# Kernel tuning notes

Measured on AMD Instinct MI355X. Metric: run time of the kernel, lower is better.

The kernel has to match this reference:

```python
import jax, jax.numpy as jnp
import numpy as np
import math

D_MODEL = 1024
NUM_HEADS = 16
HEAD_DIM = D_MODEL // NUM_HEADS  # 64
THETA = 10000.0
BATCH = 2
SEQ = 2048


def setup_inputs() -> dict:
    key = jax.random.key(0)
    ks = jax.random.split(key, 5)
    scale = 0.02
    return {
        "in_features": jax.random.normal(ks[0], (BATCH, SEQ, D_MODEL), jnp.float32),
        "q_proj": jax.random.normal(ks[1], (D_MODEL, D_MODEL), jnp.float32) * scale,
        "k_proj": jax.random.normal(ks[2], (D_MODEL, D_MODEL), jnp.float32) * scale,
        "v_proj": jax.random.normal(ks[3], (D_MODEL, D_MODEL), jnp.float32) * scale,
        "o_proj": jax.random.normal(ks[4], (D_MODEL, D_MODEL), jnp.float32) * scale,
        "token_positions": jnp.arange(SEQ, dtype=jnp.int32),
    }


def _rope(x, token_positions):
    # x: [b, h, s, head_dim]; interleaved even/odd rotation
    half = HEAD_DIM // 2
    inv_freq = 1.0 / (THETA ** (2.0 * jnp.arange(half, dtype=x.dtype) / HEAD_DIM))
    angle = token_positions.astype(x.dtype)[:, None] * inv_freq[None, :]  # [s, half]
    cos, sin = jnp.cos(angle), jnp.sin(angle)
    x_e, x_o = x[..., ::2], x[..., 1::2]
    r_e = x_e * cos - x_o * sin
    r_o = x_e * sin + x_o * cos
    # interleave back: [..., s, half, 2] -> [..., s, head_dim]
    return jnp.stack([r_e, r_o], axis=-1).reshape(x.shape)


def reference(in_features, q_proj, k_proj, v_proj, o_proj, token_positions):
    b, s, _ = in_features.shape
    # projections: weight layout is [d_out, d_in]
    Q = jnp.einsum('bsd,kd->bsk', in_features, q_proj)
    K = jnp.einsum('bsd,kd->bsk', in_features, k_proj)
    V = jnp.einsum('bsd,kd->bsk', in_features, v_proj)
    # split heads: [b, h, s, head_dim]
    Q = Q.reshape(b, s, NUM_HEADS, HEAD_DIM).transpose(0, 2, 1, 3)
    K = K.reshape(b, s, NUM_HEADS, HEAD_DIM).transpose(0, 2, 1, 3)
    V = V.reshape(b, s, NUM_HEADS, HEAD_DIM).transpose(0, 2, 1, 3)
    Q = _rope(Q, token_positions)
    K = _rope(K, token_positions)
    scores = jnp.einsum('bhnd,bhmd->bhnm', Q, K) / math.sqrt(HEAD_DIM)
    causal = jnp.tril(jnp.ones((s, s), dtype=bool))  # [s, s]
    scores = jnp.where(causal[None, None], scores, -jnp.inf)
    attn = jax.nn.softmax(scores, axis=-1)
    out = jnp.einsum('bhnm,bhmd->bhnd', attn, V)
    out = out.transpose(0, 2, 1, 3).reshape(b, s, D_MODEL)
    return jnp.einsum('bsv,dv->bsd', out, o_proj)
```

## Files before the change

kernel.cpp:

```cpp
#include <hip/hip_runtime.h>
#include <hip/hip_bf16.h>

#define D_MODEL 1024
#define NHEAD   16
#define HDIM    64
#define SEQQ    2048
#define NBATCH  2
#define MROWS   (NBATCH * SEQQ)

typedef unsigned short u16;
typedef __attribute__((ext_vector_type(8))) short short8;
typedef __attribute__((ext_vector_type(4))) short bf16x4;
typedef __attribute__((ext_vector_type(4))) float floatx4;

__device__ __forceinline__ u16 f2b(float f) {
    union { __hip_bfloat16 h; u16 u; } cv;
    cv.h = __float2bfloat16(f);
    return cv.u;
}
__device__ __forceinline__ float b2f(u16 u) {
    return __uint_as_float(((unsigned int)u) << 16);
}
__device__ __forceinline__ short8 load8(const u16* p) {
    return *reinterpret_cast<const short8*>(p);
}
__device__ __forceinline__ bf16x4 load4v(const u16* p) {
    return *reinterpret_cast<const bf16x4*>(p);
}
__device__ __forceinline__ unsigned pack2(float lo, float hi) {
    return ((unsigned)f2b(hi) << 16) | (unsigned)f2b(lo);
}
__device__ __forceinline__ void async_cp16(const void* g, void* l) {
    __builtin_amdgcn_global_load_lds(
        (const __attribute__((address_space(1))) void*)g,
        (__attribute__((address_space(3))) void*)l, 16, 0, 0);
}

__global__ void cvt_all(const float* __restrict__ X,
                        const float* __restrict__ w0, const float* __restrict__ w1,
                        const float* __restrict__ w2, const float* __restrict__ w3,
                        const int* __restrict__ pos,
                        u16* __restrict__ xo,
                        u16* __restrict__ o0, u16* __restrict__ o1,
                        u16* __restrict__ o2, u16* __restrict__ o3,
                        float2* __restrict__ tab) {
    const int z = blockIdx.y;
    const int i = blockIdx.x * 256 + threadIdx.x;
    if (z == 8) {
        if (i < SEQQ * 32) {
            const int j = i >> 11, s = i & (SEQQ - 1);
            const float p = (float)pos[s];
            const float inv = expf(-(float)j * (9.210340371976184f / 32.0f));
            float sn, cs;
            sincosf(p * inv, &sn, &cs);
            tab[i] = make_float2(cs, sn);
        }
        return;
    }
    const int n4 = (D_MODEL * D_MODEL) / 4;
    const float* in;
    u16* out;
    if (z < 4) { in = X + (size_t)z * n4 * 4;  out = xo + (size_t)z * n4 * 4; }
    else {
        in  = (z == 4) ? w0 : (z == 5) ? w1 : (z == 6) ? w2 : w3;
        out = (z == 4) ? o0 : (z == 5) ? o1 : (z == 6) ? o2 : o3;
    }
    int src = i;
    if (z == 4 || z == 5) {
        const int orow = i >> 8;
        const int g    = i & 255;
        const int irow = (orow & ~63) | (((orow & 31) << 1) | ((orow >> 5) & 1));
        src = irow * 256 + g;
    }
    float4 v = reinterpret_cast<const float4*>(in)[src];
    ushort4 o;
    o.x = f2b(v.x); o.y = f2b(v.y); o.z = f2b(v.z); o.w = f2b(v.w);
    reinterpret_cast<ushort4*>(out)[i] = o;
}

__global__ __launch_bounds__(256) void gemm_qkv(
    const u16* __restrict__ A,
    const u16* __restrict__ B0, const u16* __restrict__ B1, const u16* __restrict__ B2,
    u16* __restrict__ Qt, u16* __restrict__ Kt, u16* __restrict__ Vt,
    const float2* __restrict__ tab)
{
    const int K = D_MODEL;
    const int z = blockIdx.z;
    const u16* Bt = (z == 0) ? B0 : (z == 1 ? B1 : B2);

    __shared__ __attribute__((aligned(16))) u16 As[2][128 * 32];
    __shared__ __attribute__((aligned(16))) u16 Bs[2][128 * 32];

    const int tid  = threadIdx.x;
    const int w    = tid >> 6;
    const int lane = tid & 63;
    const int l15  = lane & 15;
    const int quad = lane >> 4;
    const int wm   = w >> 1, wn = w & 1;
    const int tm   = blockIdx.x * 128, tn = blockIdx.y * 128;

    floatx4 acc[4][4];
#pragma unroll
    for (int i = 0; i < 4; i++)
#pragma unroll
        for (int j = 0; j < 4; j++) {
            floatx4 zz = {0.f, 0.f, 0.f, 0.f};
            acc[i][j] = zz;
        }

    const int srow = lane >> 2;
    const int scol = (lane & 3) * 8;

    auto stage = [&](int buf, int k0) {
#pragma unroll
        for (int ch = w; ch < 8; ch += 4) {
            async_cp16(A  + (size_t)(tm + ch * 16 + srow) * K + k0 + scol, &As[buf][ch * 512]);
            async_cp16(Bt + (size_t)(tn + ch * 16 + srow) * K + k0 + scol, &Bs[buf][ch * 512]);
        }
    };

    stage(0, 0);

    for (int kt = 0; kt < 32; ++kt) {
        asm volatile("s_waitcnt vmcnt(0)" ::: "memory");
        __builtin_amdgcn_s_barrier();
        if (kt < 31) stage((kt + 1) & 1, (kt + 1) * 32);

        const u16* AsB = &As[kt & 1][0];
        const u16* BsB = &Bs[kt & 1][0];

        short8 af[4], bfr[4];
#pragma unroll
        for (int mi = 0; mi < 4; mi++)
            af[mi] = load8(&AsB[(wm * 64 + mi * 16 + l15) * 32 + quad * 8]);
#pragma unroll
        for (int ni = 0; ni < 4; ni++)
            bfr[ni] = load8(&BsB[(wn * 64 + ni * 16 + l15) * 32 + quad * 8]);
#pragma unroll
        for (int mi = 0; mi < 4; mi++)
#pragma unroll
            for (int ni = 0; ni < 4; ni++)
                acc[mi][ni] = __builtin_amdgcn_mfma_f32_16x16x32_bf16(af[mi], bfr[ni], acc[mi][ni], 0, 0, 0);
        __builtin_amdgcn_s_barrier();
    }

    if (z == 2) {
#pragma unroll
        for (int mi = 0; mi < 4; mi++) {
            const int r0 = tm + wm * 64 + mi * 16 + quad * 4;
            const int bb = r0 >> 11, s0 = r0 & (SEQQ - 1);
#pragma unroll
            for (int ni = 0; ni < 4; ni++) {
                const int colb = tn + wn * 64 + ni * 16 + l15;
                const int d = colb & 63, hh = colb >> 6;
                ushort4 pk;
                pk.x = f2b(acc[mi][ni][0]);
                pk.y = f2b(acc[mi][ni][1]);
                pk.z = f2b(acc[mi][ni][2]);
                pk.w = f2b(acc[mi][ni][3]);
                *reinterpret_cast<ushort4*>(
                    &Vt[(((size_t)(bb * NHEAD + hh)) * HDIM + d) * SEQQ + s0]) = pk;
            }
        }
    } else {
        const float qsc = (z == 0) ? 0.18033688011112042f : 1.0f;
        u16* Outp = (z == 0) ? Qt : Kt;
#pragma unroll
        for (int mi = 0; mi < 4; mi++) {
            const int r0 = tm + wm * 64 + mi * 16 + quad * 4;
            const int bb = r0 >> 11, s0 = r0 & (SEQQ - 1);
#pragma unroll
            for (int ni = 0; ni < 2; ni++) {
                const int p_e = tn + wn * 64 + ni * 16 + l15;
                const int hh = p_e >> 6;
                const int qq = p_e & 63;
                const float4 t01 = *reinterpret_cast<const float4*>(&tab[qq * SEQQ + s0]);
                const float4 t23 = *reinterpret_cast<const float4*>(&tab[qq * SEQQ + s0 + 2]);
                const float cs[4] = {t01.x, t01.z, t23.x, t23.z};
                const float sn[4] = {t01.y, t01.w, t23.y, t23.w};
#pragma unroll
                for (int rg = 0; rg < 4; rg++) {
                    const float e = acc[mi][ni][rg];
                    const float o = acc[mi][ni + 2][rg];
                    const float re = (e * cs[rg] - o * sn[rg]) * qsc;
                    const float ro = (e * sn[rg] + o * cs[rg]) * qsc;
                    const size_t base =
                        (((size_t)(bb * NHEAD + hh)) * SEQQ + (s0 + rg)) * HDIM;
                    Outp[base + qq]      = f2b(re);
                    Outp[base + 32 + qq] = f2b(ro);
                }
            }
        }
    }
}

__global__ __launch_bounds__(256, 4) void attn_kernel(
    const u16* __restrict__ Qt, const u16* __restrict__ Kt, const u16* __restrict__ Vt,
    u16* __restrict__ Out)
{
    const int bid = blockIdx.x;
    const int xcd = bid & 7;
    const int u   = bid >> 3;
    const int col = xcd * 4 + (u & 3);
    const int m   = u >> 2;
    int qsub;
    if      (m < 8)  qsub = 31 - m;
    else if (m < 16) qsub = m - 8;
    else if (m < 24) qsub = 39 - m;
    else             qsub = m - 16;
    const int h = col & (NHEAD - 1), b = col >> 4;

    const int tid = threadIdx.x, w = tid >> 6, lane = tid & 63;
    const int l15 = lane & 15, quad = lane >> 4;
    const size_t bh = (size_t)(b * NHEAD + h);
    const u16* Qh = Qt + bh * SEQQ * HDIM;
    const u16* Kh = Kt + bh * SEQQ * HDIM;
    const u16* Vh = Vt + bh * HDIM * SEQQ;

    __shared__ __attribute__((aligned(16))) u16 Ks[2][64 * 64];
    __shared__ __attribute__((aligned(16))) u16 Vs[2][64 * 64];

    short8 ones;
#pragma unroll
    for (int i = 0; i < 8; i++) ones[i] = (short)0x3F80;

    const int rr  = lane >> 3;
    const int swz = ((lane & 7) ^ rr) * 8;
    auto stage = [&](int buf, int tt) {
        const int k0s = tt * 64;
        async_cp16(Kh + (size_t)(k0s + w * 8 + rr) * HDIM + swz,       &Ks[buf][w * 512]);
        async_cp16(Kh + (size_t)(k0s + (w + 4) * 8 + rr) * HDIM + swz, &Ks[buf][(w + 4) * 512]);
        async_cp16(Vh + (size_t)(w * 8 + rr) * SEQQ + k0s + swz,       &Vs[buf][w * 512]);
        async_cp16(Vh + (size_t)((w + 4) * 8 + rr) * SEQQ + k0s + swz, &Vs[buf][(w + 4) * 512]);
    };

    const int s7  = l15 & 7;
    const int sw1 = ((quad)     ^ s7) * 8;
    const int sw2 = ((quad + 4) ^ s7) * 8;
    const int vo0 = (((quad >> 1)    ) ^ s7) * 8 + (quad & 1) * 4;
    const int vo1 = (((quad >> 1) + 2) ^ s7) * 8 + (quad & 1) * 4;
    const int vo2 = (((quad >> 1) + 4) ^ s7) * 8 + (quad & 1) * 4;
    const int vo3 = (((quad >> 1) + 6) ^ s7) * 8 + (quad & 1) * 4;

    const int q0w   = qsub * 64 + w * 16;
    const int tmaxp = qsub;

    short8 qf[2];
#pragma unroll
    for (int kk = 0; kk < 2; kk++)
        qf[kk] = load8(&Qh[(size_t)(q0w + l15) * HDIM + kk * 32 + quad * 8]);

    floatx4 O[4];
    floatx4 l_acc = {0.f, 0.f, 0.f, 0.f};
#pragma unroll
    for (int c = 0; c < 4; c++) { floatx4 zz = {0.f, 0.f, 0.f, 0.f}; O[c] = zz; }

    stage(0, 0);

    for (int t = 0; t <= tmaxp; ++t) {
        asm volatile("s_waitcnt vmcnt(0)" ::: "memory");
        __builtin_amdgcn_s_barrier();
        if (t < tmaxp) stage((t + 1) & 1, t + 1);

        const u16* KsB = &Ks[t & 1][0];
        const u16* VsB = &Vs[t & 1][0];
        const int k0 = t * 64;

        floatx4 S[4];
#pragma unroll
        for (int c = 0; c < 4; c++) {
            const int rowb = (c * 16 + l15) * 64;
            floatx4 zz = {0.f, 0.f, 0.f, 0.f};
            S[c] = __builtin_amdgcn_mfma_f32_16x16x32_bf16(load8(&KsB[rowb + sw1]), qf[0], zz,   0, 0, 0);
            S[c] = __builtin_amdgcn_mfma_f32_16x16x32_bf16(load8(&KsB[rowb + sw2]), qf[1], S[c], 0, 0, 0);
        }

        if (t == tmaxp) {
            const int q = q0w + l15;
#pragma unroll
            for (int c = 0; c < 4; c++)
#pragma unroll
                for (int r = 0; r < 4; r++)
                    if (k0 + c * 16 + quad * 4 + r > q) S[c][r] = -1e30f;
        }

#pragma unroll
        for (int c = 0; c < 4; c++)
#pragma unroll
            for (int r = 0; r < 4; r++)
                S[c][r] = __builtin_amdgcn_exp2f(S[c][r]);

        union { short8 v; unsigned u[4]; } pf0, pf1;
        pf0.u[0] = pack2(S[0][0], S[0][1]);
        pf0.u[1] = pack2(S[0][2], S[0][3]);
        pf0.u[2] = pack2(S[1][0], S[1][1]);
        pf0.u[3] = pack2(S[1][2], S[1][3]);
        pf1.u[0] = pack2(S[2][0], S[2][1]);
        pf1.u[1] = pack2(S[2][2], S[2][3]);
        pf1.u[2] = pack2(S[3][0], S[3][1]);
        pf1.u[3] = pack2(S[3][2], S[3][3]);

        l_acc = __builtin_amdgcn_mfma_f32_16x16x32_bf16(pf0.v, ones, l_acc, 0, 0, 0);
        l_acc = __builtin_amdgcn_mfma_f32_16x16x32_bf16(pf1.v, ones, l_acc, 0, 0, 0);

#pragma unroll
        for (int c2 = 0; c2 < 4; c2++) {
            const int rowb = (c2 * 16 + l15) * 64;
            bf16x4 a0 = load4v(&VsB[rowb + vo0]);
            bf16x4 a1 = load4v(&VsB[rowb + vo1]);
            bf16x4 a2 = load4v(&VsB[rowb + vo2]);
            bf16x4 a3 = load4v(&VsB[rowb + vo3]);
            short8 v0 = __builtin_shufflevector(a0, a1, 0, 1, 2, 3, 4, 5, 6, 7);
            short8 v1 = __builtin_shufflevector(a2, a3, 0, 1, 2, 3, 4, 5, 6, 7);
            O[c2] = __builtin_amdgcn_mfma_f32_16x16x32_bf16(pf0.v, v0, O[c2], 0, 0, 0);
            O[c2] = __builtin_amdgcn_mfma_f32_16x16x32_bf16(pf1.v, v1, O[c2], 0, 0, 0);
        }
    }

    float inv_l[4];
#pragma unroll
    for (int r = 0; r < 4; r++) inv_l[r] = 1.0f / l_acc[r];

#pragma unroll
    for (int c2 = 0; c2 < 4; c2++)
#pragma unroll
        for (int r = 0; r < 4; r++) {
            const int q    = q0w + quad * 4 + r;
            const int colo = h * HDIM + c2 * 16 + l15;
            Out[(size_t)(b * SEQQ + q) * D_MODEL + colo] = f2b(O[c2][r] * inv_l[r]);
        }
}

__global__ __launch_bounds__(256) void gemm_o(
    const u16* __restrict__ A, const u16* __restrict__ Bt, float* __restrict__ C)
{
    const int K = D_MODEL, N = D_MODEL;
    __shared__ __attribute__((aligned(16))) u16 As[2][64 * 32];
    __shared__ __attribute__((aligned(16))) u16 Bs[2][128 * 32];

    const int tid  = threadIdx.x;
    const int w    = tid >> 6;
    const int lane = tid & 63;
    const int l15  = lane & 15;
    const int quad = lane >> 4;
    const int wm   = w >> 1, wn = w & 1;
    const int tm   = blockIdx.x * 64, tn = blockIdx.y * 128;

    floatx4 acc[2][4];
#pragma unroll
    for (int i = 0; i < 2; i++)
#pragma unroll
        for (int j = 0; j < 4; j++) {
            floatx4 z = {0.f, 0.f, 0.f, 0.f};
            acc[i][j] = z;
        }

    const int srow = lane >> 2;
    const int scol = (lane & 3) * 8;

    auto stage = [&](int buf, int k0) {
#pragma unroll
        for (int ch = w; ch < 12; ch += 4) {
            if (ch < 4) async_cp16(A  + (size_t)(tm + ch * 16 + srow) * K + k0 + scol, &As[buf][ch * 512]);
            else        async_cp16(Bt + (size_t)(tn + (ch - 4) * 16 + srow) * K + k0 + scol, &Bs[buf][(ch - 4) * 512]);
        }
    };

    stage(0, 0);

    for (int kt = 0; kt < 32; ++kt) {
        asm volatile("s_waitcnt vmcnt(0)" ::: "memory");
        __builtin_amdgcn_s_barrier();
        if (kt < 31) stage((kt + 1) & 1, (kt + 1) * 32);

        const u16* AsB = &As[kt & 1][0];
        const u16* BsB = &Bs[kt & 1][0];

        short8 af[2], bfr[4];
#pragma unroll
        for (int mi = 0; mi < 2; mi++)
            af[mi] = load8(&AsB[(wm * 32 + mi * 16 + l15) * 32 + quad * 8]);
#pragma unroll
        for (int ni = 0; ni < 4; ni++)
            bfr[ni] = load8(&BsB[(wn * 64 + ni * 16 + l15) * 32 + quad * 8]);
#pragma unroll
        for (int mi = 0; mi < 2; mi++)
#pragma unroll
            for (int ni = 0; ni < 4; ni++)
                acc[mi][ni] = __builtin_amdgcn_mfma_f32_16x16x32_bf16(af[mi], bfr[ni], acc[mi][ni], 0, 0, 0);
        __builtin_amdgcn_s_barrier();
    }

#pragma unroll
    for (int mi = 0; mi < 2; mi++)
#pragma unroll
        for (int ni = 0; ni < 4; ni++)
#pragma unroll
            for (int rg = 0; rg < 4; rg++) {
                int row = tm + wm * 32 + mi * 16 + quad * 4 + rg;
                int col = tn + wn * 64 + ni * 16 + l15;
                C[(size_t)row * N + col] = acc[mi][ni][rg];
            }
}

extern "C" void kernel_launch(void* const* d_in, const int* in_sizes, int n_in,
                              void* d_out, int out_size, void* d_ws, size_t ws_size,
                              hipStream_t stream)
{
    const float* X  = (const float*)d_in[0];
    const float* Wq = (const float*)d_in[1];
    const float* Wk = (const float*)d_in[2];
    const float* Wv = (const float*)d_in[3];
    const float* Wo = (const float*)d_in[4];
    const int* tpos = (const int*)d_in[5];
    float* out = (float*)d_out;
    char* ws = (char*)d_ws;

    const size_t MB = (size_t)1 << 20;
    u16*    Xb  = (u16*)(ws + 0);
    u16*    WqB = (u16*)(ws + 8 * MB);
    u16*    WkB = (u16*)(ws + 10 * MB);
    u16*    WvB = (u16*)(ws + 12 * MB);
    u16*    WoB = (u16*)(ws + 14 * MB);
    float2* tab = (float2*)(ws + 16 * MB);
    u16*    Qt  = (u16*)(ws + 24 * MB);
    u16*    Kt  = (u16*)(ws + 32 * MB);
    u16*    Vt  = (u16*)(ws + 40 * MB);
    u16*   AOut = (u16*)(ws + 48 * MB);

    cvt_all<<<dim3(1024, 9), 256, 0, stream>>>(X, Wq, Wk, Wv, Wo, tpos,
                                               Xb, WqB, WkB, WvB, WoB, tab);

    gemm_qkv<<<dim3(32, 8, 3), 256, 0, stream>>>(Xb, WqB, WkB, WvB,
                                                 Qt, Kt, Vt, tab);
    attn_kernel<<<dim3(1024, 1, 1), 256, 0, stream>>>(Qt, Kt, Vt, AOut);
    gemm_o<<<dim3(64, 8), 256, 0, stream>>>(AOut, WoB, out);
}
```

Measured before the change: 186.3 us.

## Drop redundant GEMM barriers, pack RoPE stores, add MFMA priority hints

Removes the trailing barrier in the double-buffered QKV and output-projection GEMM loops. The barrier at the top of the next iteration already stops a wave from overwriting a buffer others are still reading. The RoPE epilogue now prefetches cos/sin table entries one group ahead. It writes each rotated even/odd pair as one packed 32-bit store, which changes the Q/K head-dim ordering identically for both, so QK dot products are unchanged. The attention loop wraps its MFMA sections in s_setprio to favour matrix issue across waves, at the cost of possible scheduling interference with the exp and pack work.

```diff
diff --git a/kernel.cpp b/kernel.cpp
--- a/kernel.cpp
+++ b/kernel.cpp
@@ -141,7 +141,6 @@
 #pragma unroll
             for (int ni = 0; ni < 4; ni++)
                 acc[mi][ni] = __builtin_amdgcn_mfma_f32_16x16x32_bf16(af[mi], bfr[ni], acc[mi][ni], 0, 0, 0);
-        __builtin_amdgcn_s_barrier();
     }
 
     if (z == 2) {
@@ -165,30 +164,35 @@
     } else {
         const float qsc = (z == 0) ? 0.18033688011112042f : 1.0f;
         u16* Outp = (z == 0) ? Qt : Kt;
-#pragma unroll
-        for (int mi = 0; mi < 4; mi++) {
+        const int hh = (tn >> 6) + wn;
+        float4 ta[2], tb[2];
+        auto ldtab = [&](int g) {
+            const int mi = g >> 1, ni = g & 1;
+            const int qq = ni * 16 + l15;
+            const int s0 = (tm + wm * 64 + mi * 16 + quad * 4) & (SEQQ - 1);
+            ta[g & 1] = *reinterpret_cast<const float4*>(&tab[qq * SEQQ + s0]);
+            tb[g & 1] = *reinterpret_cast<const float4*>(&tab[qq * SEQQ + s0 + 2]);
+        };
+        ldtab(0);
+#pragma unroll
+        for (int g = 0; g < 8; ++g) {
+            if (g < 7) ldtab(g + 1);
+            const int mi = g >> 1, ni = g & 1;
+            const int qq = ni * 16 + l15;
             const int r0 = tm + wm * 64 + mi * 16 + quad * 4;
             const int bb = r0 >> 11, s0 = r0 & (SEQQ - 1);
-#pragma unroll
-            for (int ni = 0; ni < 2; ni++) {
-                const int p_e = tn + wn * 64 + ni * 16 + l15;
-                const int hh = p_e >> 6;
-                const int qq = p_e & 63;
-                const float4 t01 = *reinterpret_cast<const float4*>(&tab[qq * SEQQ + s0]);
-                const float4 t23 = *reinterpret_cast<const float4*>(&tab[qq * SEQQ + s0 + 2]);
-                const float cs[4] = {t01.x, t01.z, t23.x, t23.z};
-                const float sn[4] = {t01.y, t01.w, t23.y, t23.w};
-#pragma unroll
-                for (int rg = 0; rg < 4; rg++) {
-                    const float e = acc[mi][ni][rg];
-                    const float o = acc[mi][ni + 2][rg];
-                    const float re = (e * cs[rg] - o * sn[rg]) * qsc;
-                    const float ro = (e * sn[rg] + o * cs[rg]) * qsc;
-                    const size_t base =
-                        (((size_t)(bb * NHEAD + hh)) * SEQQ + (s0 + rg)) * HDIM;
-                    Outp[base + qq]      = f2b(re);
-                    Outp[base + 32 + qq] = f2b(ro);
-                }
+            const float4 A4 = ta[g & 1], B4 = tb[g & 1];
+            const float cs[4] = {A4.x, A4.z, B4.x, B4.z};
+            const float sn[4] = {A4.y, A4.w, B4.y, B4.w};
+#pragma unroll
+            for (int rg = 0; rg < 4; rg++) {
+                const float e = acc[mi][ni][rg];
+                const float o = acc[mi][ni + 2][rg];
+                const unsigned val =
+                    (unsigned)f2b((e * cs[rg] - o * sn[rg]) * qsc) |
+                    ((unsigned)f2b((e * sn[rg] + o * cs[rg]) * qsc) << 16);
+                *reinterpret_cast<unsigned*>(
+                    &Outp[(((size_t)(bb * NHEAD + hh)) * SEQQ + (s0 + rg)) * HDIM + 2 * qq]) = val;
             }
         }
     }
@@ -267,6 +271,7 @@
         const int k0 = t * 64;
 
         floatx4 S[4];
+        __builtin_amdgcn_s_setprio(1);
 #pragma unroll
         for (int c = 0; c < 4; c++) {
             const int rowb = (c * 16 + l15) * 64;
@@ -274,6 +279,7 @@
             S[c] = __builtin_amdgcn_mfma_f32_16x16x32_bf16(load8(&KsB[rowb + sw1]), qf[0], zz,   0, 0, 0);
             S[c] = __builtin_amdgcn_mfma_f32_16x16x32_bf16(load8(&KsB[rowb + sw2]), qf[1], S[c], 0, 0, 0);
         }
+        __builtin_amdgcn_s_setprio(0);
 
         if (t == tmaxp) {
             const int q = q0w + l15;
@@ -300,6 +306,7 @@
         pf1.u[2] = pack2(S[3][0], S[3][1]);
         pf1.u[3] = pack2(S[3][2], S[3][3]);
 
+        __builtin_amdgcn_s_setprio(1);
         l_acc = __builtin_amdgcn_mfma_f32_16x16x32_bf16(pf0.v, ones, l_acc, 0, 0, 0);
         l_acc = __builtin_amdgcn_mfma_f32_16x16x32_bf16(pf1.v, ones, l_acc, 0, 0, 0);
 
@@ -315,6 +322,7 @@
             O[c2] = __builtin_amdgcn_mfma_f32_16x16x32_bf16(pf0.v, v0, O[c2], 0, 0, 0);
             O[c2] = __builtin_amdgcn_mfma_f32_16x16x32_bf16(pf1.v, v1, O[c2], 0, 0, 0);
         }
+        __builtin_amdgcn_s_setprio(0);
     }
 
     float inv_l[4];
@@ -388,7 +396,6 @@
 #pragma unroll
             for (int ni = 0; ni < 4; ni++)
                 acc[mi][ni] = __builtin_amdgcn_mfma_f32_16x16x32_bf16(af[mi], bfr[ni], acc[mi][ni], 0, 0, 0);
-        __builtin_amdgcn_s_barrier();
     }
 
 #pragma unroll
```

Result: no change. 184.4 us (-1.0%).
